# Kernel optimization log

Measured on AMD Instinct MI355X. Metric: run time of the kernel, lower is better.

## Reference

```python
import jax, jax.numpy as jnp
import numpy as np

B = 1048576  # number of Gaussians
EPS = 1e-8


def setup_inputs() -> dict:
    key = jax.random.key(0)
    ks = jax.random.split(key, 6)
    return {
        "loc1": jax.random.normal(ks[0], (B, 3), dtype=jnp.float32),
        "scale1": jax.random.uniform(ks[1], (B, 3), dtype=jnp.float32),
        "rot_matrix1": jax.random.normal(ks[2], (B, 3, 3), dtype=jnp.float32),
        "loc2": jax.random.normal(ks[3], (B, 3), dtype=jnp.float32),
        "scale2": jax.random.uniform(ks[4], (B, 3), dtype=jnp.float32),
        "rot_matrix2": jax.random.normal(ks[5], (B, 3, 3), dtype=jnp.float32),
    }


def reference(loc1, scale1, rot_matrix1, loc2, scale2, rot_matrix2):
    # Wasserstein-2 distance between batched 3D Gaussians.
    scale1 = jnp.clip(scale1, EPS)
    scale2 = jnp.clip(scale2, EPS)

    loc_diff2 = jnp.sum((loc1 - loc2) ** 2, axis=-1)  # [B]

    # cov2 = R2 diag(scale2) R2^T  -> [B,3,3]
    cov2 = jnp.einsum('bij,bj,bkj->bik', rot_matrix2, scale2, rot_matrix2)

    # cov2 rotated into frame 1: R1^T cov2 R1
    cov2_R1 = jnp.einsum('bji,bjk,bkl->bil', rot_matrix1, cov2, rot_matrix1)

    # E = diag(sqrt(scale1)) cov2_R1 diag(sqrt(scale1)), symmetrized
    s1_sqrt = jnp.sqrt(scale1)  # [B,3]
    E = s1_sqrt[:, :, None] * cov2_R1 * s1_sqrt[:, None, :]
    E = 0.5 * (E + jnp.swapaxes(E, -1, -2)) + EPS * jnp.eye(3, dtype=E.dtype)

    eigs = jnp.clip(jnp.linalg.eigvalsh(E), EPS)  # [B,3]
    E_sqrt_trace = jnp.sqrt(eigs).sum(axis=-1)  # [B]

    cov_w = (scale1.sum(axis=-1)
             + jnp.einsum('bii->b', cov2)
             - 2.0 * E_sqrt_trace)
    cov_w = jnp.clip(cov_w, 0.0)

    return jnp.sqrt(jnp.clip(loc_diff2 + cov_w, EPS))
```

## Files before the change

### kernel.cpp

```cpp
#include <hip/hip_runtime.h>
#include <math.h>

#define EPSF 1e-8f

__device__ __forceinline__ float tr_sqrt_eig(double a00, double a11, double a22,
                                             double a01, double a02, double a12)
{
    double q = (a00 + a11 + a22) * (1.0 / 3.0);
    double b00 = a00 - q, b11 = a11 - q, b22 = a22 - q;
    double p1 = a01 * a01 + a02 * a02 + a12 * a12;
    double p2 = b00 * b00 + b11 * b11 + b22 * b22 + 2.0 * p1;

    if (p2 <= 1e-30) {
        return 3.0f * sqrtf(fmaxf((float)q, EPSF));
    }

    double x = p2 * (1.0 / 6.0);
    double inv = rsqrt(x);
    double p = x * inv;
    double detB = b00 * (b11 * b22 - a12 * a12)
                - a01 * (a01 * b22 - a12 * a02)
                + a02 * (a01 * a12 - b11 * a02);
    double r = 0.5 * detB * (inv * inv * inv);
    r = fmin(1.0, fmax(-1.0, r));

    float phi = acosf((float)r) * (1.0f / 3.0f);
    float qf = (float)q;
    float tp = 2.0f * (float)p;
    float e0 = qf + tp * cosf(phi);
    float e1 = qf + tp * cosf(phi - 2.0943951023931953f);
    float e2 = qf + tp * cosf(phi + 2.0943951023931953f);
    return sqrtf(fmaxf(e0, EPSF)) + sqrtf(fmaxf(e1, EPSF)) + sqrtf(fmaxf(e2, EPSF));
}

__global__ __launch_bounds__(256) void wasserstein_kernel(
    const float* __restrict__ loc1, const float* __restrict__ scale1,
    const float* __restrict__ rot1, const float* __restrict__ loc2,
    const float* __restrict__ scale2, const float* __restrict__ rot2,
    float* __restrict__ out, int B)
{
    __shared__ float sR1[256 * 9];
    __shared__ float sR2[256 * 9];

    const int tid = threadIdx.x;
    const int g = blockIdx.x * 256 + tid;

    {
        const float4* r1g = (const float4*)rot1 + blockIdx.x * 576;
        const float4* r2g = (const float4*)rot2 + blockIdx.x * 576;
        float4* s1 = (float4*)sR1;
        float4* s2 = (float4*)sR2;
        s1[tid]       = r1g[tid];
        s1[tid + 256] = r1g[tid + 256];
        s2[tid]       = r2g[tid];
        s2[tid + 256] = r2g[tid + 256];
        if (tid < 64) {
            s1[tid + 512] = r1g[tid + 512];
            s2[tid + 512] = r2g[tid + 512];
        }
    }

    float a0 = loc1[3 * g], a1 = loc1[3 * g + 1], a2 = loc1[3 * g + 2];
    float b0 = loc2[3 * g], b1 = loc2[3 * g + 1], b2 = loc2[3 * g + 2];
    float s10 = fmaxf(scale1[3 * g], EPSF);
    float s11 = fmaxf(scale1[3 * g + 1], EPSF);
    float s12 = fmaxf(scale1[3 * g + 2], EPSF);
    float s20 = fmaxf(scale2[3 * g], EPSF);
    float s21 = fmaxf(scale2[3 * g + 1], EPSF);
    float s22 = fmaxf(scale2[3 * g + 2], EPSF);

    float d0 = a0 - b0, d1 = a1 - b1, d2 = a2 - b2;
    float loc_diff2 = d0 * d0 + d1 * d1 + d2 * d2;

    __syncthreads();

    const float* R2 = sR2 + 9 * tid;
    float R2r[9];
#pragma unroll
    for (int k = 0; k < 9; k++) R2r[k] = R2[k];

    float C[3][3];
    C[0][0] = R2r[0] * s20 * R2r[0] + R2r[1] * s21 * R2r[1] + R2r[2] * s22 * R2r[2];
    C[1][1] = R2r[3] * s20 * R2r[3] + R2r[4] * s21 * R2r[4] + R2r[5] * s22 * R2r[5];
    C[2][2] = R2r[6] * s20 * R2r[6] + R2r[7] * s21 * R2r[7] + R2r[8] * s22 * R2r[8];
    C[0][1] = C[1][0] = R2r[0] * s20 * R2r[3] + R2r[1] * s21 * R2r[4] + R2r[2] * s22 * R2r[5];
    C[0][2] = C[2][0] = R2r[0] * s20 * R2r[6] + R2r[1] * s21 * R2r[7] + R2r[2] * s22 * R2r[8];
    C[1][2] = C[2][1] = R2r[3] * s20 * R2r[6] + R2r[4] * s21 * R2r[7] + R2r[5] * s22 * R2r[8];
    float tr_cov2 = C[0][0] + C[1][1] + C[2][2];

    const float* R1 = sR1 + 9 * tid;
    float R1r[9];
#pragma unroll
    for (int k = 0; k < 9; k++) R1r[k] = R1[k];

    float T[3][3];
#pragma unroll
    for (int r = 0; r < 3; r++)
#pragma unroll
        for (int c = 0; c < 3; c++)
            T[r][c] = C[r][0] * R1r[c] + C[r][1] * R1r[3 + c] + C[r][2] * R1r[6 + c];

    float M[3][3];
#pragma unroll
    for (int r = 0; r < 3; r++)
#pragma unroll
        for (int c = 0; c < 3; c++)
            M[r][c] = R1r[r] * T[0][c] + R1r[3 + r] * T[1][c] + R1r[6 + r] * T[2][c];

    float ss0 = sqrtf(s10), ss1 = sqrtf(s11), ss2 = sqrtf(s12);
    double a00 = (double)(s10 * M[0][0]) + 1e-8;
    double a11 = (double)(s11 * M[1][1]) + 1e-8;
    double a22 = (double)(s12 * M[2][2]) + 1e-8;
    double a01 = (double)(0.5f * (M[0][1] + M[1][0]) * ss0 * ss1);
    double a02 = (double)(0.5f * (M[0][2] + M[2][0]) * ss0 * ss2);
    double a12 = (double)(0.5f * (M[1][2] + M[2][1]) * ss1 * ss2);

    float trs = tr_sqrt_eig(a00, a11, a22, a01, a02, a12);

    float cov_w = (s10 + s11 + s12) + tr_cov2 - 2.0f * trs;
    cov_w = fmaxf(cov_w, 0.0f);
    out[g] = sqrtf(fmaxf(loc_diff2 + cov_w, EPSF));
}

extern "C" void kernel_launch(void* const* d_in, const int* in_sizes, int n_in,
                              void* d_out, int out_size, void* d_ws, size_t ws_size,
                              hipStream_t stream) {
    const float* loc1   = (const float*)d_in[0];
    const float* scale1 = (const float*)d_in[1];
    const float* rot1   = (const float*)d_in[2];
    const float* loc2   = (const float*)d_in[3];
    const float* scale2 = (const float*)d_in[4];
    const float* rot2   = (const float*)d_in[5];
    float* out = (float*)d_out;

    int B = in_sizes[0] / 3;
    int grid = B / 256;
    wasserstein_kernel<<<grid, 256, 0, stream>>>(loc1, scale1, rot1, loc2, scale2, rot2, out, B);
}
```

Measured before the change: 147.3 us.

## Stage loc/scale through LDS with float4 loads and use sincos for eigenvalues

Loc and scale arrays, which were read with strided per-thread scalar loads, are now loaded into shared memory with coalesced float4 loads next to the rotation matrices. The rotation staging tail is reassigned to threads 192-255 so the load work is spread across threads. The eigenvalue solver replaces three cosf calls with one fast __sincosf plus the angle-addition identity, and replaces the degenerate-case branch with a clamp on p2. This cuts memory transactions and transcendental cost, at the price of more LDS use and slightly lower accuracy from the fast sincos.

```diff
diff --git a/kernel.cpp b/kernel.cpp
--- a/kernel.cpp
+++ b/kernel.cpp
@@ -10,10 +10,7 @@
     double b00 = a00 - q, b11 = a11 - q, b22 = a22 - q;
     double p1 = a01 * a01 + a02 * a02 + a12 * a12;
     double p2 = b00 * b00 + b11 * b11 + b22 * b22 + 2.0 * p1;
-
-    if (p2 <= 1e-30) {
-        return 3.0f * sqrtf(fmaxf((float)q, EPSF));
-    }
+    p2 = fmax(p2, 1e-60);
 
     double x = p2 * (1.0 / 6.0);
     double inv = rsqrt(x);
@@ -25,11 +22,13 @@
     r = fmin(1.0, fmax(-1.0, r));
 
     float phi = acosf((float)r) * (1.0f / 3.0f);
+    float c, s;
+    __sincosf(phi, &s, &c);
     float qf = (float)q;
     float tp = 2.0f * (float)p;
-    float e0 = qf + tp * cosf(phi);
-    float e1 = qf + tp * cosf(phi - 2.0943951023931953f);
-    float e2 = qf + tp * cosf(phi + 2.0943951023931953f);
+    float e0 = qf + tp * c;
+    float e1 = qf + tp * (-0.5f * c - 0.8660254037844386f * s);
+    float e2 = qf + tp * (-0.5f * c + 0.8660254037844386f * s);
     return sqrtf(fmaxf(e0, EPSF)) + sqrtf(fmaxf(e1, EPSF)) + sqrtf(fmaxf(e2, EPSF));
 }
 
@@ -39,45 +38,58 @@
     const float* __restrict__ scale2, const float* __restrict__ rot2,
     float* __restrict__ out, int B)
 {
-    __shared__ float sR1[256 * 9];
-    __shared__ float sR2[256 * 9];
+    __shared__ float sL1[768], sL2[768], sS1[768], sS2[768];
+    __shared__ float sR1[2304], sR2[2304];
 
     const int tid = threadIdx.x;
     const int g = blockIdx.x * 256 + tid;
 
     {
-        const float4* r1g = (const float4*)rot1 + blockIdx.x * 576;
-        const float4* r2g = (const float4*)rot2 + blockIdx.x * 576;
-        float4* s1 = (float4*)sR1;
-        float4* s2 = (float4*)sR2;
-        s1[tid]       = r1g[tid];
-        s1[tid + 256] = r1g[tid + 256];
-        s2[tid]       = r2g[tid];
-        s2[tid + 256] = r2g[tid + 256];
-        if (tid < 64) {
-            s1[tid + 512] = r1g[tid + 512];
-            s2[tid + 512] = r2g[tid + 512];
+        const float4* l1g = (const float4*)loc1   + blockIdx.x * 192;
+        const float4* l2g = (const float4*)loc2   + blockIdx.x * 192;
+        const float4* s1g = (const float4*)scale1 + blockIdx.x * 192;
+        const float4* s2g = (const float4*)scale2 + blockIdx.x * 192;
+        const float4* r1g = (const float4*)rot1   + blockIdx.x * 576;
+        const float4* r2g = (const float4*)rot2   + blockIdx.x * 576;
+        float4* dL1 = (float4*)sL1; float4* dL2 = (float4*)sL2;
+        float4* dS1 = (float4*)sS1; float4* dS2 = (float4*)sS2;
+        float4* dR1 = (float4*)sR1; float4* dR2 = (float4*)sR2;
+
+        if (tid < 192) {
+            dL1[tid] = l1g[tid];
+            dL2[tid] = l2g[tid];
+            dS1[tid] = s1g[tid];
+            dS2[tid] = s2g[tid];
+        }
+        dR1[tid]       = r1g[tid];
+        dR1[tid + 256] = r1g[tid + 256];
+        dR2[tid]       = r2g[tid];
+        dR2[tid + 256] = r2g[tid + 256];
+        if (tid >= 192) {
+            dR1[tid + 320] = r1g[tid + 320];
+            dR2[tid + 320] = r2g[tid + 320];
         }
     }
 
-    float a0 = loc1[3 * g], a1 = loc1[3 * g + 1], a2 = loc1[3 * g + 2];
-    float b0 = loc2[3 * g], b1 = loc2[3 * g + 1], b2 = loc2[3 * g + 2];
-    float s10 = fmaxf(scale1[3 * g], EPSF);
-    float s11 = fmaxf(scale1[3 * g + 1], EPSF);
-    float s12 = fmaxf(scale1[3 * g + 2], EPSF);
-    float s20 = fmaxf(scale2[3 * g], EPSF);
-    float s21 = fmaxf(scale2[3 * g + 1], EPSF);
-    float s22 = fmaxf(scale2[3 * g + 2], EPSF);
+    __syncthreads();
 
+    float a0 = sL1[3 * tid], a1 = sL1[3 * tid + 1], a2 = sL1[3 * tid + 2];
+    float b0 = sL2[3 * tid], b1 = sL2[3 * tid + 1], b2 = sL2[3 * tid + 2];
     float d0 = a0 - b0, d1 = a1 - b1, d2 = a2 - b2;
     float loc_diff2 = d0 * d0 + d1 * d1 + d2 * d2;
 
-    __syncthreads();
+    float s10 = fmaxf(sS1[3 * tid], EPSF);
+    float s11 = fmaxf(sS1[3 * tid + 1], EPSF);
+    float s12 = fmaxf(sS1[3 * tid + 2], EPSF);
+    float s20 = fmaxf(sS2[3 * tid], EPSF);
+    float s21 = fmaxf(sS2[3 * tid + 1], EPSF);
+    float s22 = fmaxf(sS2[3 * tid + 2], EPSF);
 
-    const float* R2 = sR2 + 9 * tid;
-    float R2r[9];
+    float R2r[9], R1r[9];
 #pragma unroll
-    for (int k = 0; k < 9; k++) R2r[k] = R2[k];
+    for (int k = 0; k < 9; k++) R2r[k] = sR2[9 * tid + k];
+#pragma unroll
+    for (int k = 0; k < 9; k++) R1r[k] = sR1[9 * tid + k];
 
     float C[3][3];
     C[0][0] = R2r[0] * s20 * R2r[0] + R2r[1] * s21 * R2r[1] + R2r[2] * s22 * R2r[2];
@@ -88,18 +100,12 @@
     C[1][2] = C[2][1] = R2r[3] * s20 * R2r[6] + R2r[4] * s21 * R2r[7] + R2r[5] * s22 * R2r[8];
     float tr_cov2 = C[0][0] + C[1][1] + C[2][2];
 
-    const float* R1 = sR1 + 9 * tid;
-    float R1r[9];
-#pragma unroll
-    for (int k = 0; k < 9; k++) R1r[k] = R1[k];
-
     float T[3][3];
 #pragma unroll
     for (int r = 0; r < 3; r++)
 #pragma unroll
         for (int c = 0; c < 3; c++)
             T[r][c] = C[r][0] * R1r[c] + C[r][1] * R1r[3 + c] + C[r][2] * R1r[6 + c];
-
     float M[3][3];
 #pragma unroll
     for (int r = 0; r < 3; r++)
```

Result: no change. 147.3 us (-0.0%).
